# Kernel tuning notes

Measured on AMD Instinct MI355X. Metric: run time of the kernel, lower is better.

Reference implementation:

```python
import jax, jax.numpy as jnp
import numpy as np

B, CIN, COUT, H, W, K = 8, 64, 64, 512, 512, 3


def setup_inputs() -> dict:
    key = jax.random.key(0)
    k1, k2, k3 = jax.random.split(key, 3)
    x = jax.random.normal(k1, (B, CIN, H, W), dtype=jnp.float32)
    w = jax.random.normal(k2, (B, CIN), dtype=jnp.float32)
    weight = jax.random.normal(k3, (COUT, CIN, K, K), dtype=jnp.float32)
    return {"x": x, "w": w, "weight": weight}


def _modulated_conv(x, w, weight):
    # x: [B, CIN, H, W], w: [B, CIN], weight: [COUT, CIN, K, K]
    b, cin, h, ww = x.shape
    cout, _, k, _ = weight.shape
    scale = 1.0 / np.sqrt(cin * k * k)  # 1 / sqrt(weight[0].numel())
    # modulate: per-sample scaling of the shared kernel -> [B, COUT, CIN, K, K]
    wm = weight[None] * w[:, None, :, None, None] * scale
    # demodulate: normalize each (sample, out-channel) filter
    d = jax.lax.rsqrt(jnp.sum(wm * wm, axis=(2, 3, 4), keepdims=True) + 1e-8)
    wm = wm * d
    # grouped conv with groups=B (up=1 -> flip_weight=True -> plain cross-correlation)
    xg = x.reshape(1, b * cin, h, ww)
    wg = wm.reshape(b * cout, cin, k, k)
    pad = k // 2
    y = jax.lax.conv_general_dilated(
        xg, wg,
        window_strides=(1, 1),
        padding=[(pad, pad), (pad, pad)],
        dimension_numbers=("NCHW", "OIHW", "NCHW"),
        feature_group_count=b,
    )
    return y.reshape(b, cout, h, ww)


def reference(x, w, weight):
    return _modulated_conv(x, w, weight)
```

## Files before the change

kernel.cpp:

```cpp
#include <hip/hip_runtime.h>
#include <math.h>

#define B 8
#define CIN 64
#define COUT 64
#define H 512
#define W 512
#define KS 3

#define TH 16
#define TW 16
#define PX 4
#define CO_T 8
#define CO_B 32
#define CI_BLK 16
#define SROW 19
#define STILE (18 * SROW)

__global__ __launch_bounds__(64) void modw_kernel(const float* __restrict__ w,
                                                  const float* __restrict__ weight,
                                                  float* __restrict__ wm) {
  int b  = blockIdx.x >> 6;
  int co = blockIdx.x & 63;
  int ci = threadIdx.x;
  const float scale = 1.0f / 24.0f;
  float wv = w[b * CIN + ci] * scale;
  const float* wp = weight + ((size_t)co * CIN + ci) * 9;
  float v[9];
  float ss = 0.f;
#pragma unroll
  for (int j = 0; j < 9; j++) {
    v[j] = wp[j] * wv;
    ss = fmaf(v[j], v[j], ss);
  }
#pragma unroll
  for (int off = 32; off > 0; off >>= 1) ss += __shfl_xor(ss, off, 64);
  float d = 1.0f / sqrtf(ss + 1e-8f);
  float* op = wm + (((size_t)b * CIN + ci) * COUT + co) * 9;
#pragma unroll
  for (int j = 0; j < 9; j++) op[j] = v[j] * d;
}

__global__ __launch_bounds__(256, 4) void conv_kernel(const float* __restrict__ x,
                                                      const float* __restrict__ wm,
                                                      float* __restrict__ y) {
  const int bx = blockIdx.x;
  const int by = blockIdx.y;
  const int bz = blockIdx.z;
  const int b   = bz >> 1;
  const int co0 = (bz & 1) * CO_B;

  const int tid  = threadIdx.x;
  const int wv   = __builtin_amdgcn_readfirstlane(tid >> 6);
  const int lane = tid & 63;
  const int tx   = lane & 3;
  const int ty   = lane >> 2;

  const int x0 = bx * TW;
  const int y0 = by * TH;
  const int co_w = co0 + wv * CO_T;

  __shared__ float sx[CI_BLK * STILE];

  float acc[CO_T][PX];
#pragma unroll
  for (int c = 0; c < CO_T; c++)
#pragma unroll
    for (int p = 0; p < PX; p++) acc[c][p] = 0.f;

  const float* xb = x + (size_t)b * CIN * H * W;

  for (int ci0 = 0; ci0 < CIN; ci0 += CI_BLK) {
    __syncthreads();
    for (int idx = tid; idx < CI_BLK * 18 * 18; idx += 256) {
      int ci  = idx / 324;
      int rem = idx - ci * 324;
      int yy  = rem / 18;
      int xx  = rem - yy * 18;
      int gy = y0 + yy - 1;
      int gx = x0 + xx - 1;
      float v = 0.f;
      if ((unsigned)gy < (unsigned)H && (unsigned)gx < (unsigned)W)
        v = xb[((size_t)(ci0 + ci) * H + gy) * W + gx];
      sx[ci * STILE + yy * SROW + xx] = v;
    }
    __syncthreads();

    for (int ci = 0; ci < CI_BLK; ci++) {
      float xw[3][6];
#pragma unroll
      for (int r = 0; r < 3; r++)
#pragma unroll
        for (int j = 0; j < 6; j++)
          xw[r][j] = sx[ci * STILE + (ty + r) * SROW + 4 * tx + j];

      const float* wp = wm + ((size_t)(b * CIN + ci0 + ci) * COUT + co_w) * 9;
#pragma unroll
      for (int c = 0; c < CO_T; c++) {
        float wgt[9];
#pragma unroll
        for (int j = 0; j < 9; j++) wgt[j] = wp[c * 9 + j];
#pragma unroll
        for (int r = 0; r < 3; r++)
#pragma unroll
          for (int kw = 0; kw < 3; kw++)
#pragma unroll
            for (int p = 0; p < PX; p++)
              acc[c][p] = fmaf(xw[r][p + kw], wgt[r * 3 + kw], acc[c][p]);
      }
    }
  }

#pragma unroll
  for (int c = 0; c < CO_T; c++) {
    float4 v = make_float4(acc[c][0], acc[c][1], acc[c][2], acc[c][3]);
    size_t o = (((size_t)b * COUT + co_w + c) * H + (y0 + ty)) * W + x0 + 4 * tx;
    *reinterpret_cast<float4*>(y + o) = v;
  }
}

extern "C" void kernel_launch(void* const* d_in, const int* in_sizes, int n_in,
                              void* d_out, int out_size, void* d_ws, size_t ws_size,
                              hipStream_t stream) {
  const float* x      = (const float*)d_in[0];
  const float* w      = (const float*)d_in[1];
  const float* weight = (const float*)d_in[2];
  float* y  = (float*)d_out;
  float* wm = (float*)d_ws;

  modw_kernel<<<B * COUT, 64, 0, stream>>>(w, weight, wm);

  dim3 grid(W / TW, H / TH, B * (COUT / CO_B));
  conv_kernel<<<grid, 256, 0, stream>>>(x, wm, y);
}
```

Before: 2.351 ms.

## Widen conv tile to 32 columns with 8 pixels per thread and precomputed staging

Doubles the spatial tile width so each thread computes 8 horizontal pixels for 8 output channels, and halves the input-channel block to keep shared memory in bounds. The shared-memory fill now uses precomputed per-thread offsets and bounds flags, replacing the per-element divisions. The compute loop processes one filter row at a time and remaps lanes so ty varies fastest. This raises arithmetic per shared-memory load and per weight load, but doubles the accumulator registers and drops the occupancy hint, which may lower occupancy.

```diff
diff --git a/kernel.cpp b/kernel.cpp
--- a/kernel.cpp
+++ b/kernel.cpp
@@ -6,16 +6,17 @@
 #define COUT 64
 #define H 512
 #define W 512
-#define KS 3
+#define HW (H * W)
 
 #define TH 16
-#define TW 16
-#define PX 4
+#define TW 32
+#define PX 8
 #define CO_T 8
 #define CO_B 32
-#define CI_BLK 16
-#define SROW 19
+#define CI_BLK 8
+#define SROW 35
 #define STILE (18 * SROW)
+#define NPOS (18 * 34)
 
 __global__ __launch_bounds__(64) void modw_kernel(const float* __restrict__ w,
                                                   const float* __restrict__ weight,
@@ -41,9 +42,9 @@
   for (int j = 0; j < 9; j++) op[j] = v[j] * d;
 }
 
-__global__ __launch_bounds__(256, 4) void conv_kernel(const float* __restrict__ x,
-                                                      const float* __restrict__ wm,
-                                                      float* __restrict__ y) {
+__global__ __launch_bounds__(256) void conv_kernel(const float* __restrict__ x,
+                                                   const float* __restrict__ wm,
+                                                   float* __restrict__ y) {
   const int bx = blockIdx.x;
   const int by = blockIdx.y;
   const int bz = blockIdx.z;
@@ -53,8 +54,8 @@
   const int tid  = threadIdx.x;
   const int wv   = __builtin_amdgcn_readfirstlane(tid >> 6);
   const int lane = tid & 63;
-  const int tx   = lane & 3;
-  const int ty   = lane >> 2;
+  const int ty   = lane & 15;
+  const int tx   = lane >> 4;
 
   const int x0 = bx * TW;
   const int y0 = by * TH;
@@ -68,54 +69,72 @@
 #pragma unroll
     for (int p = 0; p < PX; p++) acc[c][p] = 0.f;
 
-  const float* xb = x + (size_t)b * CIN * H * W;
+  const float* xb = x + (size_t)b * CIN * HW;
+
+  int  lofs[3];
+  long goff[3];
+  int  wr[3];
+  int  ld[3];
+#pragma unroll
+  for (int s = 0; s < 3; s++) {
+    int idx = tid + 256 * s;
+    int a   = idx < NPOS;
+    int yy  = idx / 34;
+    int xx  = idx - yy * 34;
+    int gy  = y0 + yy - 1;
+    int gx  = x0 + xx - 1;
+    int inb = a && ((unsigned)gy < (unsigned)H) && ((unsigned)gx < (unsigned)W);
+    wr[s]   = a;
+    ld[s]   = inb;
+    lofs[s] = yy * SROW + xx;
+    goff[s] = inb ? ((long)gy * W + gx) : 0;
+  }
 
   for (int ci0 = 0; ci0 < CIN; ci0 += CI_BLK) {
     __syncthreads();
-    for (int idx = tid; idx < CI_BLK * 18 * 18; idx += 256) {
-      int ci  = idx / 324;
-      int rem = idx - ci * 324;
-      int yy  = rem / 18;
-      int xx  = rem - yy * 18;
-      int gy = y0 + yy - 1;
-      int gx = x0 + xx - 1;
-      float v = 0.f;
-      if ((unsigned)gy < (unsigned)H && (unsigned)gx < (unsigned)W)
-        v = xb[((size_t)(ci0 + ci) * H + gy) * W + gx];
-      sx[ci * STILE + yy * SROW + xx] = v;
+#pragma unroll
+    for (int s = 0; s < 3; s++) {
+      if (wr[s]) {
+        const float* base = xb + (size_t)ci0 * HW + goff[s];
+#pragma unroll
+        for (int ci = 0; ci < CI_BLK; ci++) {
+          float v = ld[s] ? base[(size_t)ci * HW] : 0.f;
+          sx[ci * STILE + lofs[s]] = v;
+        }
+      }
     }
     __syncthreads();
 
+#pragma unroll 1
     for (int ci = 0; ci < CI_BLK; ci++) {
-      float xw[3][6];
+      const float* wp = wm + ((size_t)(b * CIN + ci0 + ci) * COUT + co_w) * 9;
+      const float* sb = sx + ci * STILE + ty * SROW + tx * PX;
 #pragma unroll
-      for (int r = 0; r < 3; r++)
+      for (int r = 0; r < 3; r++) {
+        float xr[PX + 2];
 #pragma unroll
-        for (int j = 0; j < 6; j++)
-          xw[r][j] = sx[ci * STILE + (ty + r) * SROW + 4 * tx + j];
-
-      const float* wp = wm + ((size_t)(b * CIN + ci0 + ci) * COUT + co_w) * 9;
+        for (int j = 0; j < PX + 2; j++) xr[j] = sb[r * SROW + j];
 #pragma unroll
-      for (int c = 0; c < CO_T; c++) {
-        float wgt[9];
+        for (int c = 0; c < CO_T; c++) {
 #pragma unroll
-        for (int j = 0; j < 9; j++) wgt[j] = wp[c * 9 + j];
-#pragma unroll
-        for (int r = 0; r < 3; r++)
-#pragma unroll
-          for (int kw = 0; kw < 3; kw++)
+          for (int kw = 0; kw < 3; kw++) {
+            float wgt = wp[c * 9 + r * 3 + kw];
 #pragma unroll
             for (int p = 0; p < PX; p++)
-              acc[c][p] = fmaf(xw[r][p + kw], wgt[r * 3 + kw], acc[c][p]);
+              acc[c][p] = fmaf(xr[p + kw], wgt, acc[c][p]);
+          }
+        }
       }
     }
   }
 
 #pragma unroll
   for (int c = 0; c < CO_T; c++) {
-    float4 v = make_float4(acc[c][0], acc[c][1], acc[c][2], acc[c][3]);
-    size_t o = (((size_t)b * COUT + co_w + c) * H + (y0 + ty)) * W + x0 + 4 * tx;
-    *reinterpret_cast<float4*>(y + o) = v;
+    size_t o = (((size_t)(b * COUT + co_w + c)) * H + (y0 + ty)) * W + x0 + tx * PX;
+    float4 v0 = make_float4(acc[c][0], acc[c][1], acc[c][2], acc[c][3]);
+    float4 v1 = make_float4(acc[c][4], acc[c][5], acc[c][6], acc[c][7]);
+    *reinterpret_cast<float4*>(y + o)     = v0;
+    *reinterpret_cast<float4*>(y + o + 4) = v1;
   }
 }
 
```

Measured after the change: 2.124 ms. 1.11x faster.
